# Optimization experiments

Measured on AMD Instinct MI355X. Metric: run time of the kernel, lower is better.

## Reference

```python
import jax, jax.numpy as jnp
import numpy as np

N_NODES = 100000
N_EDGES = 1600000
D_IN, D_HID, D_OUT = 64, 64, 40


def setup_inputs() -> dict:
    key = jax.random.key(0)
    ks = jax.random.split(key, 6)
    x = jax.random.normal(ks[0], (N_NODES, D_IN), dtype=jnp.float32)
    edge_index = jax.random.randint(ks[1], (2, N_EDGES), 0, N_NODES, dtype=jnp.int32)
    # Glorot-ish init for the two GCNConv linear weights
    W1 = jax.random.normal(ks[2], (D_IN, D_HID), dtype=jnp.float32) * (1.0 / np.sqrt(D_IN))
    b1 = jnp.zeros((D_HID,), dtype=jnp.float32)
    W2 = jax.random.normal(ks[3], (D_HID, D_OUT), dtype=jnp.float32) * (1.0 / np.sqrt(D_HID))
    b2 = jnp.zeros((D_OUT,), dtype=jnp.float32)
    return {"x": x, "edge_index": edge_index, "W1": W1, "b1": b1, "W2": W2, "b2": b2}


def reference(x, edge_index, W1, b1, W2, b2):
    N = x.shape[0]
    # GCNConv: add self-loops, symmetric normalization D^{-1/2}(A+I)D^{-1/2}
    loops = jnp.arange(N, dtype=edge_index.dtype)
    row = jnp.concatenate([edge_index[0], loops])  # source nodes (messages gathered here)
    col = jnp.concatenate([edge_index[1], loops])  # target nodes (scatter-add here)
    deg = jax.ops.segment_sum(jnp.ones_like(col, dtype=x.dtype), col, num_segments=N)
    dinv = jnp.where(deg > 0, jax.lax.rsqrt(deg), 0.0)
    norm = dinv[row] * dinv[col]  # [E+N]

    def gcn_conv(h, W, b):
        h = h @ W                                   # [N, d_out]
        msg = h[row] * norm[:, None]                # gather + scale  [E+N, d_out]
        return jax.ops.segment_sum(msg, col, num_segments=N) + b

    h = jax.nn.relu(gcn_conv(x, W1, b1))  # dropout is identity in eval mode
    logits = gcn_conv(h, W2, b2)
    return jax.nn.log_softmax(logits, axis=1)
```

## Files before the change

kernel.cpp:

```cpp
#include <hip/hip_runtime.h>
#include <hip/hip_bf16.h>
#include <math.h>

#define N_NODES 100000
#define N_EDGES 1600000
#define D_IN 64
#define D_HID 64
#define D_OUT 40
#define NBUCK 256
#define BSZ 391
#define BCAP 10240
#define P3_EPB 4096
#define P3_GRID ((N_EDGES + P3_EPB - 1) / P3_EPB)
#define GEMM_GRID ((N_NODES + 63) / 64)

typedef __hip_bfloat16 bf16;
typedef __attribute__((ext_vector_type(8))) short short8;
typedef __attribute__((ext_vector_type(4))) float f32x4;

__device__ __forceinline__ float bflo(unsigned int u) {
    union { unsigned int i; float f; } c; c.i = u << 16; return c.f;
}
__device__ __forceinline__ float bfhi(unsigned int u) {
    union { unsigned int i; float f; } c; c.i = u & 0xFFFF0000u; return c.f;
}
__device__ __forceinline__ unsigned short f2b(float f) {
    union { float f; unsigned int u; } c; c.f = f;
    unsigned int u = c.u + 0x7FFFu + ((c.u >> 16) & 1u);
    return (unsigned short)(u >> 16);
}
__device__ __forceinline__ float i8f(unsigned int w, int b) {
    return (float)((int)(w << ((3 - b) * 8)) >> 24);
}
__device__ __forceinline__ unsigned int qpack(float v0, float v1, float v2,
                                              float v3, float qs) {
    int q0 = __float2int_rn(v0 * qs), q1 = __float2int_rn(v1 * qs);
    int q2 = __float2int_rn(v2 * qs), q3 = __float2int_rn(v3 * qs);
    return (unsigned int)(q0 & 255) | ((unsigned int)(q1 & 255) << 8) |
           ((unsigned int)(q2 & 255) << 16) | ((unsigned int)(q3 & 255) << 24);
}

__global__ __launch_bounds__(256) void k_zero(int* __restrict__ p, int n) {
    int i = blockIdx.x * 256 + threadIdx.x;
    if (i < n) p[i] = 0;
}

__global__ __launch_bounds__(256) void k_cnt(const int* __restrict__ col,
                                             int* __restrict__ bcnt_p) {
    __shared__ int hist[NBUCK];
    hist[threadIdx.x] = 0;
    __syncthreads();
    for (int e = blockIdx.x * 256 + threadIdx.x; e < N_EDGES; e += 256 * 256) {
        unsigned int c = (unsigned int)col[e];
        atomicAdd(&hist[c / 391u], 1);
    }
    __syncthreads();
    int hv = hist[threadIdx.x];
    if (hv) atomicAdd(&bcnt_p[threadIdx.x * 16], hv);
}

__global__ __launch_bounds__(256) void k_scan256(const int* __restrict__ bcnt_p,
                                                 int* __restrict__ fill_p,
                                                 int* __restrict__ bucket_base) {
    __shared__ int sm[256];
    int t = threadIdx.x;
    int v = bcnt_p[t * 16];
    sm[t] = v;
    __syncthreads();
    for (int off = 1; off < 256; off <<= 1) {
        int u = (t >= off) ? sm[t - off] : 0;
        __syncthreads();
        sm[t] += u;
        __syncthreads();
    }
    int excl = sm[t] - v;
    bucket_base[t] = excl;
    fill_p[t * 16] = excl;
    if (t == 255) bucket_base[256] = sm[255];
}

__global__ __launch_bounds__(256) void k_place(const int* __restrict__ ei,
                                               int* __restrict__ fill_p,
                                               int* __restrict__ part) {
    __shared__ int cnt_l[NBUCK];
    __shared__ int base_l[NBUCK];
    cnt_l[threadIdx.x] = 0;
    __syncthreads();
    int e0 = blockIdx.x * P3_EPB;
    unsigned int meta[16];
#pragma unroll
    for (int k = 0; k < 16; k++) {
        int e = e0 + k * 256 + threadIdx.x;
        if (e < N_EDGES) {
            unsigned int c = (unsigned int)ei[N_EDGES + e];
            unsigned int b = c / 391u;
            unsigned int lc = c - b * 391u;
            unsigned int slot = atomicAdd(&cnt_l[b], 1);
            meta[k] = (b << 21) | (lc << 12) | slot;
        } else meta[k] = 0xFFFFFFFFu;
    }
    __syncthreads();
    int cv = cnt_l[threadIdx.x];
    if (cv) base_l[threadIdx.x] = atomicAdd(&fill_p[threadIdx.x * 16], cv);
    __syncthreads();
#pragma unroll
    for (int k = 0; k < 16; k++) {
        if (meta[k] != 0xFFFFFFFFu) {
            int e = e0 + k * 256 + threadIdx.x;
            unsigned int b = meta[k] >> 21;
            unsigned int lc = (meta[k] >> 12) & 0x1FFu;
            unsigned int slot = meta[k] & 0xFFFu;
            unsigned int r = (unsigned int)ei[e];
            part[base_l[b] + slot] = (int)((lc << 17) | r);
        }
    }
}

__global__ __launch_bounds__(256) void k_build(const int* __restrict__ part,
                                               const int* __restrict__ bucket_base,
                                               int* __restrict__ start,
                                               int* __restrict__ nkv,
                                               float* __restrict__ dinv,
                                               int* __restrict__ csr) {
    __shared__ int deg_l[392];
    __shared__ int excl_l[392];
    int tid = threadIdx.x;
    int b = blockIdx.x;
    int base = bucket_base[b], end = bucket_base[b + 1];
    int m = end - base;
    int cbase = b * BCAP;
    for (int i = tid; i < 392; i += 256) deg_l[i] = 0;
    __syncthreads();
    for (int i = tid; i < m; i += 256)
        atomicAdd(&deg_l[(unsigned int)part[base + i] >> 17], 1);
    __syncthreads();
    if (tid < 64) {
        int carry = 0;
        for (int ch = 0; ch < 7; ch++) {
            int idx = ch * 64 + tid;
            int val = (idx < 392) ? ((deg_l[idx] + 7) & ~7) : 0;
            int incl = val;
#pragma unroll
            for (int off = 1; off < 64; off <<= 1) {
                int u = __shfl_up(incl, off, 64);
                if (tid >= off) incl += u;
            }
            if (idx < 392) excl_l[idx] = carry + incl - val;
            carry += __shfl(incl, 63, 64);
        }
    }
    __syncthreads();
    int v0 = b * BSZ;
    for (int vl = tid; vl < BSZ; vl += 256) {
        int v = v0 + vl;
        if (v < N_NODES) {
            int d = deg_l[vl];
            start[v] = cbase + excl_l[vl];
            nkv[v] = (d + 7) >> 3;
            dinv[v] = rsqrtf((float)d + 1.0f);
        }
    }
    __syncthreads();
    for (int j = tid; j < 392 * 8; j += 256) {
        int vl = j >> 3, sl = j & 7;
        int d = deg_l[vl];
        int pc = ((d + 7) & ~7) - d;
        if (sl < pc) csr[cbase + excl_l[vl] + d + sl] = N_NODES;
    }
    __syncthreads();
    for (int i = tid; i < 392; i += 256) deg_l[i] = 0;
    __syncthreads();
    for (int i = tid; i < m; i += 256) {
        unsigned int p = (unsigned int)part[base + i];
        unsigned int lc = p >> 17;
        int s = atomicAdd(&deg_l[lc], 1);
        csr[cbase + excl_l[lc] + s] = (int)(p & 0x1FFFFu);
    }
}

__global__ __launch_bounds__(256) void k_prep(const float* __restrict__ W1,
                                              const float* __restrict__ W2,
                                              unsigned short* __restrict__ wp1,
                                              unsigned short* __restrict__ wp2,
                                              unsigned int* __restrict__ gb8,
                                              unsigned int* __restrict__ g2q,
                                              float* __restrict__ scale1,
                                              float* __restrict__ scale2) {
    int tid = threadIdx.x;
    if (tid < 16) gb8[(size_t)N_NODES * 16 + tid] = 0;
    else if (tid < 32) g2q[(size_t)N_NODES * 16 + (tid - 16)] = 0;
    else if (tid == 32) { scale1[N_NODES] = 0.f; scale2[N_NODES] = 0.f; }
    for (int i = tid; i < 4096; i += 256) {
        int e = i & 7, lane = (i >> 3) & 63, t = i >> 9;
        int kk = t >> 2, jt = t & 3;
        int row = kk * 32 + (lane >> 4) * 8 + e;
        int col = jt * 16 + (lane & 15);
        wp1[i] = f2b(W1[row * 64 + col]);
    }
    for (int i = tid; i < 3072; i += 256) {
        int e = i & 7, lane = (i >> 3) & 63, t = i >> 9;
        int kk = t / 3, jt = t - kk * 3;
        int row = kk * 32 + (lane >> 4) * 8 + e;
        int col = jt * 16 + (lane & 15);
        wp2[i] = (col < 40) ? f2b(W2[row * 40 + col]) : (unsigned short)0;
    }
}

__global__ __launch_bounds__(256) void k_gemm1m(const float* __restrict__ x,
                                                const short8* __restrict__ wp,
                                                const float* __restrict__ dinv,
                                                unsigned int* __restrict__ gb8,
                                                float* __restrict__ scale1) {
    int lane = threadIdx.x & 63;
    int wid = threadIdx.x >> 6;
    int node0 = (blockIdx.x * 4 + wid) * 16;
    if (node0 >= N_NODES) return;
    int vr = node0 + (lane & 15);
    if (vr >= N_NODES) vr = N_NODES - 1;
    int kg = lane >> 4;
    const float* px = x + (size_t)vr * 64 + kg * 8;
    short8 b0, b1;
    {
        float4 f0 = *(const float4*)px;
        float4 f1 = *(const float4*)(px + 4);
        b0[0] = (short)f2b(f0.x); b0[1] = (short)f2b(f0.y);
        b0[2] = (short)f2b(f0.z); b0[3] = (short)f2b(f0.w);
        b0[4] = (short)f2b(f1.x); b0[5] = (short)f2b(f1.y);
        b0[6] = (short)f2b(f1.z); b0[7] = (short)f2b(f1.w);
        float4 g0 = *(const float4*)(px + 32);
        float4 g1 = *(const float4*)(px + 36);
        b1[0] = (short)f2b(g0.x); b1[1] = (short)f2b(g0.y);
        b1[2] = (short)f2b(g0.z); b1[3] = (short)f2b(g0.w);
        b1[4] = (short)f2b(g1.x); b1[5] = (short)f2b(g1.y);
        b1[6] = (short)f2b(g1.z); b1[7] = (short)f2b(g1.w);
    }
    f32x4 acc[4];
#pragma unroll
    for (int jt = 0; jt < 4; jt++) acc[jt] = (f32x4){0.f, 0.f, 0.f, 0.f};
#pragma unroll
    for (int jt = 0; jt < 4; jt++) {
        acc[jt] = __builtin_amdgcn_mfma_f32_16x16x32_bf16(
            wp[(0 * 4 + jt) * 64 + lane], b0, acc[jt], 0, 0, 0);
        acc[jt] = __builtin_amdgcn_mfma_f32_16x16x32_bf16(
            wp[(1 * 4 + jt) * 64 + lane], b1, acc[jt], 0, 0, 0);
    }
    float d = dinv[vr];
    float mv[4][4];
    float amax = 0.f;
#pragma unroll
    for (int jt = 0; jt < 4; jt++)
#pragma unroll
        for (int i = 0; i < 4; i++) {
            float val = acc[jt][i] * d;
            mv[jt][i] = val;
            amax = fmaxf(amax, fabsf(val));
        }
    amax = fmaxf(amax, __shfl_xor(amax, 16, 64));
    amax = fmaxf(amax, __shfl_xor(amax, 32, 64));
    float qs = (amax > 0.f) ? 127.f / amax : 0.f;
    if (kg == 0) scale1[vr] = amax * (1.f / 127.f);
    unsigned int* gp = gb8 + (size_t)vr * 16 + kg;
#pragma unroll
    for (int jt = 0; jt < 4; jt++)
        gp[jt * 4] = qpack(mv[jt][0], mv[jt][1], mv[jt][2], mv[jt][3], qs);
}

__global__ __launch_bounds__(256) void k_gemm2m(const unsigned short* __restrict__ hb,
                                                const short8* __restrict__ wp,
                                                const float* __restrict__ dinv,
                                                unsigned int* __restrict__ g2q,
                                                float* __restrict__ scale2) {
    int lane = threadIdx.x & 63;
    int wid = threadIdx.x >> 6;
    int node0 = (blockIdx.x * 4 + wid) * 16;
    if (node0 >= N_NODES) return;
    int vr = node0 + (lane & 15);
    if (vr >= N_NODES) vr = N_NODES - 1;
    int kg = lane >> 4;
    const short8* h8 = (const short8*)hb;
    short8 b0 = h8[(size_t)vr * 8 + kg];
    short8 b1 = h8[(size_t)vr * 8 + 4 + kg];
    f32x4 acc[3];
#pragma unroll
    for (int jt = 0; jt < 3; jt++) acc[jt] = (f32x4){0.f, 0.f, 0.f, 0.f};
#pragma unroll
    for (int jt = 0; jt < 3; jt++) {
        acc[jt] = __builtin_amdgcn_mfma_f32_16x16x32_bf16(
            wp[(0 * 3 + jt) * 64 + lane], b0, acc[jt], 0, 0, 0);
        acc[jt] = __builtin_amdgcn_mfma_f32_16x16x32_bf16(
            wp[(1 * 3 + jt) * 64 + lane], b1, acc[jt], 0, 0, 0);
    }
    float d = dinv[vr];
    bool v2 = (kg < 2);
    float mv[3][4];
    float amax = 0.f;
#pragma unroll
    for (int jt = 0; jt < 3; jt++)
#pragma unroll
        for (int i = 0; i < 4; i++) {
            float val = acc[jt][i] * d;
            mv[jt][i] = val;
            if (jt < 2 || v2) amax = fmaxf(amax, fabsf(val));
        }
    amax = fmaxf(amax, __shfl_xor(amax, 16, 64));
    amax = fmaxf(amax, __shfl_xor(amax, 32, 64));
    float qs = (amax > 0.f) ? 127.f / amax : 0.f;
    if (kg == 0) scale2[vr] = amax * (1.f / 127.f);
    unsigned int* gp = g2q + (size_t)vr * 16;
    gp[0 * 4 + kg] = qpack(mv[0][0], mv[0][1], mv[0][2], mv[0][3], qs);
    gp[1 * 4 + kg] = qpack(mv[1][0], mv[1][1], mv[1][2], mv[1][3], qs);
    gp[8 + kg] = v2 ? qpack(mv[2][0], mv[2][1], mv[2][2], mv[2][3], qs) : 0u;
    gp[12 + kg] = 0u;
}

__global__ __launch_bounds__(256) void k_agg1(const int* __restrict__ csr,
                                              const int* __restrict__ start,
                                              const int* __restrict__ nkv,
                                              const unsigned int* __restrict__ gb8,
                                              const float* __restrict__ scale1,
                                              const float* __restrict__ dinv,
                                              const float* __restrict__ b1,
                                              unsigned short* __restrict__ hb) {
    int lane = threadIdx.x & 63;
    int g = lane >> 3;
    int lq = lane & 7;
    int v = blockIdx.x * 4 + (threadIdx.x >> 6);
    int s = start[v] + g;
    int nk = nkv[v];
    float a0=0.f,a1=0.f,a2=0.f,a3=0.f,a4=0.f,a5=0.f,a6=0.f,a7=0.f;
    if (g == 0) {
        float sc = scale1[v];
        uint2 u = *(const uint2*)(gb8 + (size_t)v * 16 + lq * 2);
        a0 = fmaf(i8f(u.x,0), sc, a0); a1 = fmaf(i8f(u.x,1), sc, a1);
        a2 = fmaf(i8f(u.x,2), sc, a2); a3 = fmaf(i8f(u.x,3), sc, a3);
        a4 = fmaf(i8f(u.y,0), sc, a4); a5 = fmaf(i8f(u.y,1), sc, a5);
        a6 = fmaf(i8f(u.y,2), sc, a6); a7 = fmaf(i8f(u.y,3), sc, a7);
    }
#pragma unroll 2
    for (int k = 0; k < nk; k++) {
        int r = csr[s + k * 8];
        float sc = scale1[r];
        uint2 u = *(const uint2*)(gb8 + (size_t)r * 16 + lq * 2);
        a0 = fmaf(i8f(u.x,0), sc, a0); a1 = fmaf(i8f(u.x,1), sc, a1);
        a2 = fmaf(i8f(u.x,2), sc, a2); a3 = fmaf(i8f(u.x,3), sc, a3);
        a4 = fmaf(i8f(u.y,0), sc, a4); a5 = fmaf(i8f(u.y,1), sc, a5);
        a6 = fmaf(i8f(u.y,2), sc, a6); a7 = fmaf(i8f(u.y,3), sc, a7);
    }
#pragma unroll
    for (int o = 8; o < 64; o <<= 1) {
        a0 += __shfl_xor(a0, o, 64); a1 += __shfl_xor(a1, o, 64);
        a2 += __shfl_xor(a2, o, 64); a3 += __shfl_xor(a3, o, 64);
        a4 += __shfl_xor(a4, o, 64); a5 += __shfl_xor(a5, o, 64);
        a6 += __shfl_xor(a6, o, 64); a7 += __shfl_xor(a7, o, 64);
    }
    float d = dinv[v];
    float4 bb0 = ((const float4*)b1)[lq * 2];
    float4 bb1 = ((const float4*)b1)[lq * 2 + 1];
    float h0 = fmaxf(d * a0 + bb0.x, 0.f), h1 = fmaxf(d * a1 + bb0.y, 0.f);
    float h2 = fmaxf(d * a2 + bb0.z, 0.f), h3 = fmaxf(d * a3 + bb0.w, 0.f);
    float h4 = fmaxf(d * a4 + bb1.x, 0.f), h5 = fmaxf(d * a5 + bb1.y, 0.f);
    float h6 = fmaxf(d * a6 + bb1.z, 0.f), h7 = fmaxf(d * a7 + bb1.w, 0.f);
    if (g == 0) {
        uint4 o;
        o.x = (unsigned int)f2b(h0) | ((unsigned int)f2b(h1) << 16);
        o.y = (unsigned int)f2b(h2) | ((unsigned int)f2b(h3) << 16);
        o.z = (unsigned int)f2b(h4) | ((unsigned int)f2b(h5) << 16);
        o.w = (unsigned int)f2b(h6) | ((unsigned int)f2b(h7) << 16);
        *(uint4*)(hb + (size_t)v * 64 + lq * 8) = o;
    }
}

__global__ __launch_bounds__(256) void k_agg2(const int* __restrict__ csr,
                                              const int* __restrict__ start,
                                              const int* __restrict__ nkv,
                                              const unsigned int* __restrict__ g2q,
                                              const float* __restrict__ scale2,
                                              const float* __restrict__ dinv,
                                              const float* __restrict__ b2v,
                                              float* __restrict__ out) {
    int lane = threadIdx.x & 63;
    int g = lane >> 3;
    int lq = lane & 7;
    int v = blockIdx.x * 4 + (threadIdx.x >> 6);
    int s = start[v] + g;
    int nk = nkv[v];
    bool act = (lq < 5);
    float a0=0.f,a1=0.f,a2=0.f,a3=0.f,a4=0.f,a5=0.f,a6=0.f,a7=0.f;
    if (g == 0) {
        float sc = scale2[v];
        uint2 u = *(const uint2*)(g2q + (size_t)v * 16 + lq * 2);
        a0 = fmaf(i8f(u.x,0), sc, a0); a1 = fmaf(i8f(u.x,1), sc, a1);
        a2 = fmaf(i8f(u.x,2), sc, a2); a3 = fmaf(i8f(u.x,3), sc, a3);
        a4 = fmaf(i8f(u.y,0), sc, a4); a5 = fmaf(i8f(u.y,1), sc, a5);
        a6 = fmaf(i8f(u.y,2), sc, a6); a7 = fmaf(i8f(u.y,3), sc, a7);
    }
#pragma unroll 2
    for (int k = 0; k < nk; k++) {
        int r = csr[s + k * 8];
        float sc = scale2[r];
        uint2 u = *(const uint2*)(g2q + (size_t)r * 16 + lq * 2);
        a0 = fmaf(i8f(u.x,0), sc, a0); a1 = fmaf(i8f(u.x,1), sc, a1);
        a2 = fmaf(i8f(u.x,2), sc, a2); a3 = fmaf(i8f(u.x,3), sc, a3);
        a4 = fmaf(i8f(u.y,0), sc, a4); a5 = fmaf(i8f(u.y,1), sc, a5);
        a6 = fmaf(i8f(u.y,2), sc, a6); a7 = fmaf(i8f(u.y,3), sc, a7);
    }
#pragma unroll
    for (int o = 8; o < 64; o <<= 1) {
        a0 += __shfl_xor(a0, o, 64); a1 += __shfl_xor(a1, o, 64);
        a2 += __shfl_xor(a2, o, 64); a3 += __shfl_xor(a3, o, 64);
        a4 += __shfl_xor(a4, o, 64); a5 += __shfl_xor(a5, o, 64);
        a6 += __shfl_xor(a6, o, 64); a7 += __shfl_xor(a7, o, 64);
    }
    float d = dinv[v];
    float4 bb0 = act ? ((const float4*)b2v)[lq * 2] : make_float4(0.f,0.f,0.f,0.f);
    float4 bb1 = act ? ((const float4*)b2v)[lq * 2 + 1] : make_float4(0.f,0.f,0.f,0.f);
    float l0 = act ? d * a0 + bb0.x : -INFINITY;
    float l1 = act ? d * a1 + bb0.y : -INFINITY;
    float l2 = act ? d * a2 + bb0.z : -INFINITY;
    float l3 = act ? d * a3 + bb0.w : -INFINITY;
    float l4 = act ? d * a4 + bb1.x : -INFINITY;
    float l5 = act ? d * a5 + bb1.y : -INFINITY;
    float l6 = act ? d * a6 + bb1.z : -INFINITY;
    float l7 = act ? d * a7 + bb1.w : -INFINITY;
    float m = fmaxf(fmaxf(fmaxf(l0, l1), fmaxf(l2, l3)),
                    fmaxf(fmaxf(l4, l5), fmaxf(l6, l7)));
#pragma unroll
    for (int o = 1; o < 8; o <<= 1) m = fmaxf(m, __shfl_xor(m, o, 64));
    float ex = act ? (__expf(l0 - m) + __expf(l1 - m) + __expf(l2 - m) +
                      __expf(l3 - m) + __expf(l4 - m) + __expf(l5 - m) +
                      __expf(l6 - m) + __expf(l7 - m)) : 0.f;
#pragma unroll
    for (int o = 1; o < 8; o <<= 1) ex += __shfl_xor(ex, o, 64);
    float lse = m + logf(ex);
    if (g == 0 && act) {
        float* op = out + (size_t)v * 40 + lq * 8;
        *(float4*)op = make_float4(l0 - lse, l1 - lse, l2 - lse, l3 - lse);
        *(float4*)(op + 4) = make_float4(l4 - lse, l5 - lse, l6 - lse, l7 - lse);
    }
}

extern "C" void kernel_launch(void* const* d_in, const int* in_sizes, int n_in,
                              void* d_out, int out_size, void* d_ws, size_t ws_size,
                              hipStream_t stream) {
    const float* x  = (const float*)d_in[0];
    const int*   ei = (const int*)d_in[1];
    const float* W1 = (const float*)d_in[2];
    const float* b1 = (const float*)d_in[3];
    const float* W2 = (const float*)d_in[4];
    const float* b2 = (const float*)d_in[5];
    float* out = (float*)d_out;

    const int N = N_NODES;
    int*   part  = (int*)d_ws;
    int*   csr   = part + N_EDGES;
    int*   start = csr + NBUCK * BCAP;
    int*   nkv   = start + N;
    int*   bcnt  = nkv + N;
    int*   fill  = bcnt + 4096;
    int*   bbase = fill + 4096;
    float* dinv  = (float*)(bbase + 260);
    float* scale1 = dinv + N;
    float* scale2 = scale1 + N + 4;
    unsigned short* hb  = (unsigned short*)(scale2 + N + 4);
    unsigned int* gb8 = (unsigned int*)(hb + (size_t)N * 64);
    unsigned int* g2q = gb8 + (size_t)(N + 1) * 16;
    unsigned short* wp1 = (unsigned short*)(g2q + (size_t)(N + 1) * 16);
    unsigned short* wp2 = wp1 + 4096;

    k_zero<<<16, 256, 0, stream>>>(bcnt, 4096);
    k_prep<<<1, 256, 0, stream>>>(W1, W2, wp1, wp2, gb8, g2q, scale1, scale2);
    k_cnt<<<256, 256, 0, stream>>>(ei + N_EDGES, bcnt);
    k_scan256<<<1, 256, 0, stream>>>(bcnt, fill, bbase);
    k_place<<<P3_GRID, 256, 0, stream>>>(ei, fill, part);
    k_build<<<NBUCK, 256, 0, stream>>>(part, bbase, start, nkv, dinv, csr);
    k_gemm1m<<<GEMM_GRID, 256, 0, stream>>>(x, (const short8*)wp1, dinv, gb8, scale1);
    k_agg1<<<N / 4, 256, 0, stream>>>(csr, start, nkv, gb8, scale1, dinv, b1, hb);
    k_gemm2m<<<GEMM_GRID, 256, 0, stream>>>(hb, (const short8*)wp2, dinv, g2q, scale2);
    k_agg2<<<N / 4, 256, 0, stream>>>(csr, start, nkv, g2q, scale2, dinv, b2, out);
}
```

Baseline: 254.3 us.

## Drop bucket count/scan passes and process two nodes per wavefront in aggregation

The bucketed edge partition now writes into fixed-capacity per-bucket regions (bucket*BCAP plus an atomic fill offset), so the separate count and scan kernels are removed and k_build reads each bucket's size straight from the fill counters. Both aggregation kernels now have each wavefront handle two destination nodes, interleaving their neighbor gathers to expose more independent memory loads, and the grid is halved. The cost is doubled accumulator registers, possible lower occupancy, and load imbalance when the two nodes' degrees differ. It also relies on no bucket exceeding BCAP entries, which the old layout did not need for the partition buffer.

```diff
diff --git a/kernel.cpp b/kernel.cpp
--- a/kernel.cpp
+++ b/kernel.cpp
@@ -13,6 +13,7 @@
 #define P3_EPB 4096
 #define P3_GRID ((N_EDGES + P3_EPB - 1) / P3_EPB)
 #define GEMM_GRID ((N_NODES + 63) / 64)
+#define AGG_GRID (N_NODES / 8)
 
 typedef __hip_bfloat16 bf16;
 typedef __attribute__((ext_vector_type(8))) short short8;
@@ -43,40 +44,6 @@
 __global__ __launch_bounds__(256) void k_zero(int* __restrict__ p, int n) {
     int i = blockIdx.x * 256 + threadIdx.x;
     if (i < n) p[i] = 0;
-}
-
-__global__ __launch_bounds__(256) void k_cnt(const int* __restrict__ col,
-                                             int* __restrict__ bcnt_p) {
-    __shared__ int hist[NBUCK];
-    hist[threadIdx.x] = 0;
-    __syncthreads();
-    for (int e = blockIdx.x * 256 + threadIdx.x; e < N_EDGES; e += 256 * 256) {
-        unsigned int c = (unsigned int)col[e];
-        atomicAdd(&hist[c / 391u], 1);
-    }
-    __syncthreads();
-    int hv = hist[threadIdx.x];
-    if (hv) atomicAdd(&bcnt_p[threadIdx.x * 16], hv);
-}
-
-__global__ __launch_bounds__(256) void k_scan256(const int* __restrict__ bcnt_p,
-                                                 int* __restrict__ fill_p,
-                                                 int* __restrict__ bucket_base) {
-    __shared__ int sm[256];
-    int t = threadIdx.x;
-    int v = bcnt_p[t * 16];
-    sm[t] = v;
-    __syncthreads();
-    for (int off = 1; off < 256; off <<= 1) {
-        int u = (t >= off) ? sm[t - off] : 0;
-        __syncthreads();
-        sm[t] += u;
-        __syncthreads();
-    }
-    int excl = sm[t] - v;
-    bucket_base[t] = excl;
-    fill_p[t * 16] = excl;
-    if (t == 255) bucket_base[256] = sm[255];
 }
 
 __global__ __launch_bounds__(256) void k_place(const int* __restrict__ ei,
@@ -101,7 +68,8 @@
     }
     __syncthreads();
     int cv = cnt_l[threadIdx.x];
-    if (cv) base_l[threadIdx.x] = atomicAdd(&fill_p[threadIdx.x * 16], cv);
+    if (cv) base_l[threadIdx.x] = threadIdx.x * BCAP +
+                                  atomicAdd(&fill_p[threadIdx.x * 16], cv);
     __syncthreads();
 #pragma unroll
     for (int k = 0; k < 16; k++) {
@@ -117,7 +85,7 @@
 }
 
 __global__ __launch_bounds__(256) void k_build(const int* __restrict__ part,
-                                               const int* __restrict__ bucket_base,
+                                               const int* __restrict__ fill_p,
                                                int* __restrict__ start,
                                                int* __restrict__ nkv,
                                                float* __restrict__ dinv,
@@ -126,9 +94,8 @@
     __shared__ int excl_l[392];
     int tid = threadIdx.x;
     int b = blockIdx.x;
-    int base = bucket_base[b], end = bucket_base[b + 1];
-    int m = end - base;
-    int cbase = b * BCAP;
+    int m = fill_p[b * 16];
+    int base = b * BCAP;
     for (int i = tid; i < 392; i += 256) deg_l[i] = 0;
     __syncthreads();
     for (int i = tid; i < m; i += 256)
@@ -155,7 +122,7 @@
         int v = v0 + vl;
         if (v < N_NODES) {
             int d = deg_l[vl];
-            start[v] = cbase + excl_l[vl];
+            start[v] = base + excl_l[vl];
             nkv[v] = (d + 7) >> 3;
             dinv[v] = rsqrtf((float)d + 1.0f);
         }
@@ -165,7 +132,7 @@
         int vl = j >> 3, sl = j & 7;
         int d = deg_l[vl];
         int pc = ((d + 7) & ~7) - d;
-        if (sl < pc) csr[cbase + excl_l[vl] + d + sl] = N_NODES;
+        if (sl < pc) csr[base + excl_l[vl] + d + sl] = N_NODES;
     }
     __syncthreads();
     for (int i = tid; i < 392; i += 256) deg_l[i] = 0;
@@ -174,7 +141,7 @@
         unsigned int p = (unsigned int)part[base + i];
         unsigned int lc = p >> 17;
         int s = atomicAdd(&deg_l[lc], 1);
-        csr[cbase + excl_l[lc] + s] = (int)(p & 0x1FFFFu);
+        csr[base + excl_l[lc] + s] = (int)(p & 0x1FFFFu);
     }
 }
 
@@ -324,21 +291,45 @@
     int lane = threadIdx.x & 63;
     int g = lane >> 3;
     int lq = lane & 7;
-    int v = blockIdx.x * 4 + (threadIdx.x >> 6);
-    int s = start[v] + g;
-    int nk = nkv[v];
+    int v0 = (blockIdx.x * 4 + (threadIdx.x >> 6)) * 2;
+    int v1 = v0 + 1;
+    int s0 = start[v0] + g, s1 = start[v1] + g;
+    int n0 = nkv[v0], n1 = nkv[v1];
     float a0=0.f,a1=0.f,a2=0.f,a3=0.f,a4=0.f,a5=0.f,a6=0.f,a7=0.f;
+    float c0=0.f,c1=0.f,c2=0.f,c3=0.f,c4=0.f,c5=0.f,c6=0.f,c7=0.f;
     if (g == 0) {
-        float sc = scale1[v];
-        uint2 u = *(const uint2*)(gb8 + (size_t)v * 16 + lq * 2);
-        a0 = fmaf(i8f(u.x,0), sc, a0); a1 = fmaf(i8f(u.x,1), sc, a1);
-        a2 = fmaf(i8f(u.x,2), sc, a2); a3 = fmaf(i8f(u.x,3), sc, a3);
-        a4 = fmaf(i8f(u.y,0), sc, a4); a5 = fmaf(i8f(u.y,1), sc, a5);
-        a6 = fmaf(i8f(u.y,2), sc, a6); a7 = fmaf(i8f(u.y,3), sc, a7);
-    }
+        float sA = scale1[v0];
+        uint2 uA = *(const uint2*)(gb8 + (size_t)v0 * 16 + lq * 2);
+        a0 = fmaf(i8f(uA.x,0), sA, a0); a1 = fmaf(i8f(uA.x,1), sA, a1);
+        a2 = fmaf(i8f(uA.x,2), sA, a2); a3 = fmaf(i8f(uA.x,3), sA, a3);
+        a4 = fmaf(i8f(uA.y,0), sA, a4); a5 = fmaf(i8f(uA.y,1), sA, a5);
+        a6 = fmaf(i8f(uA.y,2), sA, a6); a7 = fmaf(i8f(uA.y,3), sA, a7);
+        float sB = scale1[v1];
+        uint2 uB = *(const uint2*)(gb8 + (size_t)v1 * 16 + lq * 2);
+        c0 = fmaf(i8f(uB.x,0), sB, c0); c1 = fmaf(i8f(uB.x,1), sB, c1);
+        c2 = fmaf(i8f(uB.x,2), sB, c2); c3 = fmaf(i8f(uB.x,3), sB, c3);
+        c4 = fmaf(i8f(uB.y,0), sB, c4); c5 = fmaf(i8f(uB.y,1), sB, c5);
+        c6 = fmaf(i8f(uB.y,2), sB, c6); c7 = fmaf(i8f(uB.y,3), sB, c7);
+    }
+    int nc = (n0 < n1) ? n0 : n1;
 #pragma unroll 2
-    for (int k = 0; k < nk; k++) {
-        int r = csr[s + k * 8];
+    for (int k = 0; k < nc; k++) {
+        int r0 = csr[s0 + k * 8];
+        int r1 = csr[s1 + k * 8];
+        float sA = scale1[r0], sB = scale1[r1];
+        uint2 uA = *(const uint2*)(gb8 + (size_t)r0 * 16 + lq * 2);
+        uint2 uB = *(const uint2*)(gb8 + (size_t)r1 * 16 + lq * 2);
+        a0 = fmaf(i8f(uA.x,0), sA, a0); a1 = fmaf(i8f(uA.x,1), sA, a1);
+        a2 = fmaf(i8f(uA.x,2), sA, a2); a3 = fmaf(i8f(uA.x,3), sA, a3);
+        a4 = fmaf(i8f(uA.y,0), sA, a4); a5 = fmaf(i8f(uA.y,1), sA, a5);
+        a6 = fmaf(i8f(uA.y,2), sA, a6); a7 = fmaf(i8f(uA.y,3), sA, a7);
+        c0 = fmaf(i8f(uB.x,0), sB, c0); c1 = fmaf(i8f(uB.x,1), sB, c1);
+        c2 = fmaf(i8f(uB.x,2), sB, c2); c3 = fmaf(i8f(uB.x,3), sB, c3);
+        c4 = fmaf(i8f(uB.y,0), sB, c4); c5 = fmaf(i8f(uB.y,1), sB, c5);
+        c6 = fmaf(i8f(uB.y,2), sB, c6); c7 = fmaf(i8f(uB.y,3), sB, c7);
+    }
+    for (int k = nc; k < n0; k++) {
+        int r = csr[s0 + k * 8];
         float sc = scale1[r];
         uint2 u = *(const uint2*)(gb8 + (size_t)r * 16 + lq * 2);
         a0 = fmaf(i8f(u.x,0), sc, a0); a1 = fmaf(i8f(u.x,1), sc, a1);
@@ -346,21 +337,39 @@
         a4 = fmaf(i8f(u.y,0), sc, a4); a5 = fmaf(i8f(u.y,1), sc, a5);
         a6 = fmaf(i8f(u.y,2), sc, a6); a7 = fmaf(i8f(u.y,3), sc, a7);
     }
+    for (int k = nc; k < n1; k++) {
+        int r = csr[s1 + k * 8];
+        float sc = scale1[r];
+        uint2 u = *(const uint2*)(gb8 + (size_t)r * 16 + lq * 2);
+        c0 = fmaf(i8f(u.x,0), sc, c0); c1 = fmaf(i8f(u.x,1), sc, c1);
+        c2 = fmaf(i8f(u.x,2), sc, c2); c3 = fmaf(i8f(u.x,3), sc, c3);
+        c4 = fmaf(i8f(u.y,0), sc, c4); c5 = fmaf(i8f(u.y,1), sc, c5);
+        c6 = fmaf(i8f(u.y,2), sc, c6); c7 = fmaf(i8f(u.y,3), sc, c7);
+    }
 #pragma unroll
     for (int o = 8; o < 64; o <<= 1) {
         a0 += __shfl_xor(a0, o, 64); a1 += __shfl_xor(a1, o, 64);
         a2 += __shfl_xor(a2, o, 64); a3 += __shfl_xor(a3, o, 64);
         a4 += __shfl_xor(a4, o, 64); a5 += __shfl_xor(a5, o, 64);
         a6 += __shfl_xor(a6, o, 64); a7 += __shfl_xor(a7, o, 64);
-    }
+        c0 += __shfl_xor(c0, o, 64); c1 += __shfl_xor(c1, o, 64);
+        c2 += __shfl_xor(c2, o, 64); c3 += __shfl_xor(c3, o, 64);
+        c4 += __shfl_xor(c4, o, 64); c5 += __shfl_xor(c5, o, 64);
+        c6 += __shfl_xor(c6, o, 64); c7 += __shfl_xor(c7, o, 64);
+    }
+    bool hi = (lane >= 32);
+    int v = hi ? v1 : v0;
     float d = dinv[v];
+    float e0 = hi ? c0 : a0, e1 = hi ? c1 : a1, e2 = hi ? c2 : a2;
+    float e3 = hi ? c3 : a3, e4 = hi ? c4 : a4, e5 = hi ? c5 : a5;
+    float e6 = hi ? c6 : a6, e7 = hi ? c7 : a7;
     float4 bb0 = ((const float4*)b1)[lq * 2];
     float4 bb1 = ((const float4*)b1)[lq * 2 + 1];
-    float h0 = fmaxf(d * a0 + bb0.x, 0.f), h1 = fmaxf(d * a1 + bb0.y, 0.f);
-    float h2 = fmaxf(d * a2 + bb0.z, 0.f), h3 = fmaxf(d * a3 + bb0.w, 0.f);
-    float h4 = fmaxf(d * a4 + bb1.x, 0.f), h5 = fmaxf(d * a5 + bb1.y, 0.f);
-    float h6 = fmaxf(d * a6 + bb1.z, 0.f), h7 = fmaxf(d * a7 + bb1.w, 0.f);
-    if (g == 0) {
+    float h0 = fmaxf(d * e0 + bb0.x, 0.f), h1 = fmaxf(d * e1 + bb0.y, 0.f);
+    float h2 = fmaxf(d * e2 + bb0.z, 0.f), h3 = fmaxf(d * e3 + bb0.w, 0.f);
+    float h4 = fmaxf(d * e4 + bb1.x, 0.f), h5 = fmaxf(d * e5 + bb1.y, 0.f);
+    float h6 = fmaxf(d * e6 + bb1.z, 0.f), h7 = fmaxf(d * e7 + bb1.w, 0.f);
+    if (g == 0 || g == 4) {
         uint4 o;
         o.x = (unsigned int)f2b(h0) | ((unsigned int)f2b(h1) << 16);
         o.y = (unsigned int)f2b(h2) | ((unsigned int)f2b(h3) << 16);
@@ -381,22 +390,45 @@
     int lane = threadIdx.x & 63;
     int g = lane >> 3;
     int lq = lane & 7;
-    int v = blockIdx.x * 4 + (threadIdx.x >> 6);
-    int s = start[v] + g;
-    int nk = nkv[v];
-    bool act = (lq < 5);
+    int v0 = (blockIdx.x * 4 + (threadIdx.x >> 6)) * 2;
+    int v1 = v0 + 1;
+    int s0 = start[v0] + g, s1 = start[v1] + g;
+    int n0 = nkv[v0], n1 = nkv[v1];
     float a0=0.f,a1=0.f,a2=0.f,a3=0.f,a4=0.f,a5=0.f,a6=0.f,a7=0.f;
+    float c0=0.f,c1=0.f,c2=0.f,c3=0.f,c4=0.f,c5=0.f,c6=0.f,c7=0.f;
     if (g == 0) {
-        float sc = scale2[v];
-        uint2 u = *(const uint2*)(g2q + (size_t)v * 16 + lq * 2);
-        a0 = fmaf(i8f(u.x,0), sc, a0); a1 = fmaf(i8f(u.x,1), sc, a1);
-        a2 = fmaf(i8f(u.x,2), sc, a2); a3 = fmaf(i8f(u.x,3), sc, a3);
-        a4 = fmaf(i8f(u.y,0), sc, a4); a5 = fmaf(i8f(u.y,1), sc, a5);
-        a6 = fmaf(i8f(u.y,2), sc, a6); a7 = fmaf(i8f(u.y,3), sc, a7);
-    }
+        float sA = scale2[v0];
+        uint2 uA = *(const uint2*)(g2q + (size_t)v0 * 16 + lq * 2);
+        a0 = fmaf(i8f(uA.x,0), sA, a0); a1 = fmaf(i8f(uA.x,1), sA, a1);
+        a2 = fmaf(i8f(uA.x,2), sA, a2); a3 = fmaf(i8f(uA.x,3), sA, a3);
+        a4 = fmaf(i8f(uA.y,0), sA, a4); a5 = fmaf(i8f(uA.y,1), sA, a5);
+        a6 = fmaf(i8f(uA.y,2), sA, a6); a7 = fmaf(i8f(uA.y,3), sA, a7);
+        float sB = scale2[v1];
+        uint2 uB = *(const uint2*)(g2q + (size_t)v1 * 16 + lq * 2);
+        c0 = fmaf(i8f(uB.x,0), sB, c0); c1 = fmaf(i8f(uB.x,1), sB, c1);
+        c2 = fmaf(i8f(uB.x,2), sB, c2); c3 = fmaf(i8f(uB.x,3), sB, c3);
+        c4 = fmaf(i8f(uB.y,0), sB, c4); c5 = fmaf(i8f(uB.y,1), sB, c5);
+        c6 = fmaf(i8f(uB.y,2), sB, c6); c7 = fmaf(i8f(uB.y,3), sB, c7);
+    }
+    int nc = (n0 < n1) ? n0 : n1;
 #pragma unroll 2
-    for (int k = 0; k < nk; k++) {
-        int r = csr[s + k * 8];
+    for (int k = 0; k < nc; k++) {
+        int r0 = csr[s0 + k * 8];
+        int r1 = csr[s1 + k * 8];
+        float sA = scale2[r0], sB = scale2[r1];
+        uint2 uA = *(const uint2*)(g2q + (size_t)r0 * 16 + lq * 2);
+        uint2 uB = *(const uint2*)(g2q + (size_t)r1 * 16 + lq * 2);
+        a0 = fmaf(i8f(uA.x,0), sA, a0); a1 = fmaf(i8f(uA.x,1), sA, a1);
+        a2 = fmaf(i8f(uA.x,2), sA, a2); a3 = fmaf(i8f(uA.x,3), sA, a3);
+        a4 = fmaf(i8f(uA.y,0), sA, a4); a5 = fmaf(i8f(uA.y,1), sA, a5);
+        a6 = fmaf(i8f(uA.y,2), sA, a6); a7 = fmaf(i8f(uA.y,3), sA, a7);
+        c0 = fmaf(i8f(uB.x,0), sB, c0); c1 = fmaf(i8f(uB.x,1), sB, c1);
+        c2 = fmaf(i8f(uB.x,2), sB, c2); c3 = fmaf(i8f(uB.x,3), sB, c3);
+        c4 = fmaf(i8f(uB.y,0), sB, c4); c5 = fmaf(i8f(uB.y,1), sB, c5);
+        c6 = fmaf(i8f(uB.y,2), sB, c6); c7 = fmaf(i8f(uB.y,3), sB, c7);
+    }
+    for (int k = nc; k < n0; k++) {
+        int r = csr[s0 + k * 8];
         float sc = scale2[r];
         uint2 u = *(const uint2*)(g2q + (size_t)r * 16 + lq * 2);
         a0 = fmaf(i8f(u.x,0), sc, a0); a1 = fmaf(i8f(u.x,1), sc, a1);
@@ -404,24 +436,43 @@
         a4 = fmaf(i8f(u.y,0), sc, a4); a5 = fmaf(i8f(u.y,1), sc, a5);
         a6 = fmaf(i8f(u.y,2), sc, a6); a7 = fmaf(i8f(u.y,3), sc, a7);
     }
+    for (int k = nc; k < n1; k++) {
+        int r = csr[s1 + k * 8];
+        float sc = scale2[r];
+        uint2 u = *(const uint2*)(g2q + (size_t)r * 16 + lq * 2);
+        c0 = fmaf(i8f(u.x,0), sc, c0); c1 = fmaf(i8f(u.x,1), sc, c1);
+        c2 = fmaf(i8f(u.x,2), sc, c2); c3 = fmaf(i8f(u.x,3), sc, c3);
+        c4 = fmaf(i8f(u.y,0), sc, c4); c5 = fmaf(i8f(u.y,1), sc, c5);
+        c6 = fmaf(i8f(u.y,2), sc, c6); c7 = fmaf(i8f(u.y,3), sc, c7);
+    }
 #pragma unroll
     for (int o = 8; o < 64; o <<= 1) {
         a0 += __shfl_xor(a0, o, 64); a1 += __shfl_xor(a1, o, 64);
         a2 += __shfl_xor(a2, o, 64); a3 += __shfl_xor(a3, o, 64);
         a4 += __shfl_xor(a4, o, 64); a5 += __shfl_xor(a5, o, 64);
         a6 += __shfl_xor(a6, o, 64); a7 += __shfl_xor(a7, o, 64);
-    }
+        c0 += __shfl_xor(c0, o, 64); c1 += __shfl_xor(c1, o, 64);
+        c2 += __shfl_xor(c2, o, 64); c3 += __shfl_xor(c3, o, 64);
+        c4 += __shfl_xor(c4, o, 64); c5 += __shfl_xor(c5, o, 64);
+        c6 += __shfl_xor(c6, o, 64); c7 += __shfl_xor(c7, o, 64);
+    }
+    bool hi = (lane >= 32);
+    int v = hi ? v1 : v0;
     float d = dinv[v];
+    float e0 = hi ? c0 : a0, e1 = hi ? c1 : a1, e2 = hi ? c2 : a2;
+    float e3 = hi ? c3 : a3, e4 = hi ? c4 : a4, e5 = hi ? c5 : a5;
+    float e6 = hi ? c6 : a6, e7 = hi ? c7 : a7;
+    bool act = (lq < 5);
     float4 bb0 = act ? ((const float4*)b2v)[lq * 2] : make_float4(0.f,0.f,0.f,0.f);
     float4 bb1 = act ? ((const float4*)b2v)[lq * 2 + 1] : make_float4(0.f,0.f,0.f,0.f);
-    float l0 = act ? d * a0 + bb0.x : -INFINITY;
-    float l1 = act ? d * a1 + bb0.y : -INFINITY;
-    float l2 = act ? d * a2 + bb0.z : -INFINITY;
-    float l3 = act ? d * a3 + bb0.w : -INFINITY;
-    float l4 = act ? d * a4 + bb1.x : -INFINITY;
-    float l5 = act ? d * a5 + bb1.y : -INFINITY;
-    float l6 = act ? d * a6 + bb1.z : -INFINITY;
-    float l7 = act ? d * a7 + bb1.w : -INFINITY;
+    float l0 = act ? d * e0 + bb0.x : -INFINITY;
+    float l1 = act ? d * e1 + bb0.y : -INFINITY;
+    float l2 = act ? d * e2 + bb0.z : -INFINITY;
+    float l3 = act ? d * e3 + bb0.w : -INFINITY;
+    float l4 = act ? d * e4 + bb1.x : -INFINITY;
+    float l5 = act ? d * e5 + bb1.y : -INFINITY;
+    float l6 = act ? d * e6 + bb1.z : -INFINITY;
+    float l7 = act ? d * e7 + bb1.w : -INFINITY;
     float m = fmaxf(fmaxf(fmaxf(l0, l1), fmaxf(l2, l3)),
                     fmaxf(fmaxf(l4, l5), fmaxf(l6, l7)));
 #pragma unroll
@@ -432,7 +483,7 @@
 #pragma unroll
     for (int o = 1; o < 8; o <<= 1) ex += __shfl_xor(ex, o, 64);
     float lse = m + logf(ex);
-    if (g == 0 && act) {
+    if ((g == 0 || g == 4) && act) {
         float* op = out + (size_t)v * 40 + lq * 8;
         *(float4*)op = make_float4(l0 - lse, l1 - lse, l2 - lse, l3 - lse);
         *(float4*)(op + 4) = make_float4(l4 - lse, l5 - lse, l6 - lse, l7 - lse);
@@ -452,13 +503,11 @@
 
     const int N = N_NODES;
     int*   part  = (int*)d_ws;
-    int*   csr   = part + N_EDGES;
+    int*   csr   = part + NBUCK * BCAP;
     int*   start = csr + NBUCK * BCAP;
     int*   nkv   = start + N;
-    int*   bcnt  = nkv + N;
-    int*   fill  = bcnt + 4096;
-    int*   bbase = fill + 4096;
-    float* dinv  = (float*)(bbase + 260);
+    int*   fill  = nkv + N;
+    float* dinv  = (float*)(fill + 4096);
     float* scale1 = dinv + N;
     float* scale2 = scale1 + N + 4;
     unsigned short* hb  = (unsigned short*)(scale2 + N + 4);
@@ -467,14 +516,12 @@
     unsigned short* wp1 = (unsigned short*)(g2q + (size_t)(N + 1) * 16);
     unsigned short* wp2 = wp1 + 4096;
 
-    k_zero<<<16, 256, 0, stream>>>(bcnt, 4096);
+    k_zero<<<16, 256, 0, stream>>>(fill, 4096);
     k_prep<<<1, 256, 0, stream>>>(W1, W2, wp1, wp2, gb8, g2q, scale1, scale2);
-    k_cnt<<<256, 256, 0, stream>>>(ei + N_EDGES, bcnt);
-    k_scan256<<<1, 256, 0, stream>>>(bcnt, fill, bbase);
     k_place<<<P3_GRID, 256, 0, stream>>>(ei, fill, part);
-    k_build<<<NBUCK, 256, 0, stream>>>(part, bbase, start, nkv, dinv, csr);
+    k_build<<<NBUCK, 256, 0, stream>>>(part, fill, start, nkv, dinv, csr);
     k_gemm1m<<<GEMM_GRID, 256, 0, stream>>>(x, (const short8*)wp1, dinv, gb8, scale1);
-    k_agg1<<<N / 4, 256, 0, stream>>>(csr, start, nkv, gb8, scale1, dinv, b1, hb);
+    k_agg1<<<AGG_GRID, 256, 0, stream>>>(csr, start, nkv, gb8, scale1, dinv, b1, hb);
     k_gemm2m<<<GEMM_GRID, 256, 0, stream>>>(hb, (const short8*)wp2, dinv, g2q, scale2);
-    k_agg2<<<N / 4, 256, 0, stream>>>(csr, start, nkv, g2q, scale2, dinv, b2, out);
-}
+    k_agg2<<<AGG_GRID, 256, 0, stream>>>(csr, start, nkv, g2q, scale2, dinv, b2, out);
+}
```

Measured after the change: 239.7 us. 5.7% less time.
